# Performance work log

Measured on AMD Instinct MI355X. Metric: run time of the kernel, lower is better.

The kernel has to match this reference:

```python
import jax, jax.numpy as jnp
import numpy as np

B, L, DIM, H = 1, 2048, 1536, 24
HD = DIM // H  # head_dim = 64
EPS = 1e-6


def _rmsnorm(x, g):
    # RMSNorm over last dim with learnable scale (matches RMSNorm with elementwise_affine=True)
    return x * jax.lax.rsqrt(jnp.mean(x * x, axis=-1, keepdims=True) + EPS) * g


def setup_inputs() -> dict:
    key = jax.random.key(0)
    ks = jax.random.split(key, 4)
    s = 0.02
    return {
        "x": jax.random.normal(ks[0], (B, L, DIM), jnp.float32),
        "w_qkv": jax.random.normal(ks[1], (3 * DIM, DIM), jnp.float32) * s,
        "b_qkv": jnp.zeros((3 * DIM,), jnp.float32),
        "w_proj": jax.random.normal(ks[2], (DIM, DIM), jnp.float32) * s,
        "b_proj": jnp.zeros((DIM,), jnp.float32),
        "g_q": jnp.ones((HD,), jnp.float32),
        "g_k": jnp.ones((HD,), jnp.float32),
    }


def reference(x, w_qkv, b_qkv, w_proj, b_proj, g_q, g_k):
    Bb, Ll, C = x.shape
    # fused QKV projection: [B,L,C] -> [B,L,3C] -> [B,L,3,H,HD]
    qkv = (x @ w_qkv.T + b_qkv).reshape(Bb, Ll, 3, H, HD)
    q, k, v = qkv[:, :, 0], qkv[:, :, 1], qkv[:, :, 2]  # each [B,L,H,HD]
    # per-head RMS norm on q/k (qk_norm='rms')
    q = _rmsnorm(q, g_q)
    k = _rmsnorm(k, g_k)
    # scaled dot-product attention (torch SDPA default scale = 1/sqrt(head_dim))
    scale = 1.0 / np.sqrt(HD).astype(np.float32)
    scores = jnp.einsum('bqhd,bkhd->bhqk', q, k) * scale  # [B,H,L,L]
    attn = jax.nn.softmax(scores, axis=-1)
    o = jnp.einsum('bhqk,bkhd->bqhd', attn, v).reshape(Bb, Ll, C)
    # output projection
    return o @ w_proj.T + b_proj
```

## Files before the change

### kernel.cpp

```cpp
#include <hip/hip_runtime.h>
#include <stdint.h>

#define L_SEQ 2048
#define DIM 1536
#define NH 24
#define HD 64
#define NQKV 4608

typedef unsigned short u16;
typedef __attribute__((ext_vector_type(4))) float f32x4;
typedef __attribute__((ext_vector_type(8))) short bf16x8;
typedef __attribute__((ext_vector_type(4))) u16 u16x4;
typedef __attribute__((ext_vector_type(8))) u16 u16x8;

__device__ __forceinline__ u16 f2bf(float f) {
  unsigned u = __builtin_bit_cast(unsigned, f);
  u += 0x7fffu + ((u >> 16) & 1u);
  return (u16)(u >> 16);
}
__device__ __forceinline__ float b2f(u16 u) {
  return __builtin_bit_cast(float, (unsigned)u << 16);
}
__device__ __forceinline__ unsigned cvt_pk_bf16(float lo, float hi) {
  unsigned r;
  asm("v_cvt_pk_bf16_f32 %0, %1, %2" : "=v"(r) : "v"(lo), "v"(hi));
  return r;
}

__device__ __forceinline__ void gload_lds16(const void* g, void* lds) {
  __builtin_amdgcn_global_load_lds(
      (const __attribute__((address_space(1))) unsigned int*)g,
      (__attribute__((address_space(3))) unsigned int*)lds, 16, 0, 0);
}

__global__ __launch_bounds__(256) void cast3_kernel(const float* __restrict__ x,
                                                    const float* __restrict__ wq,
                                                    const float* __restrict__ wp,
                                                    u16* __restrict__ out) {
  const int n1 = (L_SEQ * DIM) / 4;
  const int n2 = (NQKV * DIM) / 4;
  const int n3 = (DIM * DIM) / 4;
  const int tot = n1 + n2 + n3;
  for (int i = blockIdx.x * 256 + threadIdx.x; i < tot; i += gridDim.x * 256) {
    const f32x4* src;
    int j;
    if (i < n1) {
      src = (const f32x4*)x;
      j = i;
    } else if (i < n1 + n2) {
      src = (const f32x4*)wq;
      j = i - n1;
    } else {
      src = (const f32x4*)wp;
      j = i - n1 - n2;
    }
    f32x4 v = src[j];
    u16x4 o;
    o.x = f2bf(v.x);
    o.y = f2bf(v.y);
    o.z = f2bf(v.z);
    o.w = f2bf(v.w);
    ((u16x4*)out)[i] = o;
  }
}

template <int WRITE_BF16, int BN>
__global__ __launch_bounds__(256) void gemm_bt(const u16* __restrict__ A,
                                               const u16* __restrict__ B,
                                               const float* __restrict__ bias,
                                               void* __restrict__ Cout,
                                               int M, int N, int K) {
  constexpr int NT = BN / 64 * 2;
  __shared__ u16 As[2][128 * 32];
  __shared__ u16 Bs[2][BN * 32];
  const int mb = M >> 7;
  const int f = (int)blockIdx.x;
  const int f2 = (f & 7) * ((int)gridDim.x >> 3) + (f >> 3);
  const int bx = f2 / mb;
  const int by = f2 % mb;
  const int tid = threadIdx.x;
  const int lane = tid & 63;
  const int l4 = lane & 15;
  const int wv = tid >> 6;
  const int wr = wv >> 1, wc = wv & 1;

  f32x4 acc[4][NT];
#pragma unroll
  for (int i = 0; i < 4; i++)
#pragma unroll
    for (int j = 0; j < NT; j++) acc[i][j] = (f32x4)(0.0f);

  const int e0 = tid * 8;
  const int r0 = e0 >> 5, c0 = e0 & 31;
  const u16* Ag0 = A + (size_t)(by * 128 + r0) * K + c0;
  const u16* Ag1 = A + (size_t)(by * 128 + r0 + 64) * K + c0;
  const u16* Bg0 = B + (size_t)(bx * BN + r0) * K + c0;
  const u16* Bg1 = B + (size_t)(bx * BN + r0 + 64) * K + c0;
  const int kc = (lane >> 4) * 8;
  const int wb = wv * 1024;

  gload_lds16(Ag0, (char*)As[0] + wb);
  gload_lds16(Ag1, (char*)As[0] + wb + 4096);
  gload_lds16(Bg0, (char*)Bs[0] + wb);
  if (BN == 128) gload_lds16(Bg1, (char*)Bs[0] + wb + 4096);
  __syncthreads();

  int cur = 0;
  for (int k0 = 0; k0 < K; k0 += 32) {
    const int nxt = cur ^ 1;
    if (k0 + 32 < K) {
      gload_lds16(Ag0 + k0 + 32, (char*)As[nxt] + wb);
      gload_lds16(Ag1 + k0 + 32, (char*)As[nxt] + wb + 4096);
      gload_lds16(Bg0 + k0 + 32, (char*)Bs[nxt] + wb);
      if (BN == 128) gload_lds16(Bg1 + k0 + 32, (char*)Bs[nxt] + wb + 4096);
    }
    const u16* Asc = As[cur];
    const u16* Bsc = Bs[cur];
    bf16x8 af[4], bfr[NT];
#pragma unroll
    for (int mt = 0; mt < 4; mt++)
      af[mt] = *(const bf16x8*)&Asc[(wr * 64 + mt * 16 + l4) * 32 + kc];
#pragma unroll
    for (int nt = 0; nt < NT; nt++)
      bfr[nt] = *(const bf16x8*)&Bsc[(wc * (BN / 2) + nt * 16 + l4) * 32 + kc];
#pragma unroll
    for (int mt = 0; mt < 4; mt++)
#pragma unroll
      for (int nt = 0; nt < NT; nt++)
        acc[mt][nt] = __builtin_amdgcn_mfma_f32_16x16x32_bf16(af[mt], bfr[nt],
                                                              acc[mt][nt], 0, 0, 0);
    __syncthreads();
    cur = nxt;
  }

  const int colb = bx * BN + wc * (BN / 2) + l4;
  const int rowb = by * 128 + wr * 64 + ((lane >> 4) << 2);
#pragma unroll
  for (int nt = 0; nt < NT; nt++) {
    const int col = colb + nt * 16;
    const float bv = bias[col];
#pragma unroll
    for (int mt = 0; mt < 4; mt++) {
#pragma unroll
      for (int r = 0; r < 4; r++) {
        const int row = rowb + mt * 16 + r;
        float v = acc[mt][nt][r] + bv;
        if (WRITE_BF16)
          ((u16*)Cout)[(size_t)row * N + col] = f2bf(v);
        else
          ((float*)Cout)[(size_t)row * N + col] = v;
      }
    }
  }
}

__global__ __launch_bounds__(256) void qkvnorm_kernel(const u16* __restrict__ qkv,
                                                      const float* __restrict__ gq,
                                                      const float* __restrict__ gk,
                                                      u16* __restrict__ Qh,
                                                      u16* __restrict__ Kh,
                                                      u16* __restrict__ Vt) {
  const int h = blockIdx.y;
  const int lblk = blockIdx.x * 64;
  const int tid = threadIdx.x;
  const int lane = tid & 63, wv = tid >> 6;
  __shared__ u16 vt[64][64];
  const float gqv = gq[lane] * 0.125f * 1.44269504088896f;
  const float gkv = gk[lane];
#pragma unroll 1
  for (int i = 0; i < 16; i++) {
    const int l = lblk + wv * 16 + i;
    const size_t base = (size_t)l * NQKV + h * HD + lane;
    const float q = b2f(qkv[base]);
    const float k = b2f(qkv[base + DIM]);
    float sq = q * q, sk = k * k;
#pragma unroll
    for (int m = 32; m; m >>= 1) {
      sq += __shfl_xor(sq, m);
      sk += __shfl_xor(sk, m);
    }
    const float rq = rsqrtf(sq * (1.0f / 64.0f) + 1e-6f);
    const float rk = rsqrtf(sk * (1.0f / 64.0f) + 1e-6f);
    const size_t ho = ((size_t)h * L_SEQ + l) * HD + lane;
    Qh[ho] = f2bf(q * rq * gqv);
    Kh[ho] = f2bf(k * rk * gkv);
    vt[wv * 16 + i][lane] = qkv[base + 2 * DIM];
  }
  __syncthreads();
  const int d = tid >> 2;
  const int cb = (tid & 3) * 16;
  u16* dst = Vt + ((size_t)h * HD + d) * L_SEQ + lblk + cb;
#pragma unroll
  for (int j0 = 0; j0 < 4; j0++) {
    u16x4 o;
    o.x = vt[cb + j0 * 4 + 0][d];
    o.y = vt[cb + j0 * 4 + 1][d];
    o.z = vt[cb + j0 * 4 + 2][d];
    o.w = vt[cb + j0 * 4 + 3][d];
    *(u16x4*)(dst + j0 * 4) = o;
  }
}

__global__ __launch_bounds__(256) void flash_kernel(const u16* __restrict__ Qh,
                                                    const u16* __restrict__ Kh,
                                                    const u16* __restrict__ Vt,
                                                    u16* __restrict__ O) {
  const int f = (int)blockIdx.y * (L_SEQ / 64) + (int)blockIdx.x;
  const int f2 = (f & 7) * 96 + (f >> 3);
  const int h = f2 >> 5;
  const int qblk = (f2 & 31) * 64;
  const int tid = threadIdx.x;
  const int lane = tid & 63, wv = tid >> 6;
  __shared__ u16 Ks[64][64];
  __shared__ u16 Vs[64][64];
  __shared__ u16 Ps[4][16][64];

  const int l4 = lane & 15;
  const int g = lane >> 4;
  const int kc = g * 8;
  const int swz = (l4 & 7) << 3;

  const int qrow = qblk + wv * 16 + l4;
  const u16* Qp = Qh + ((size_t)h * L_SEQ + qrow) * HD;
  const bf16x8 qf0 = *(const bf16x8*)(Qp + kc);
  const bf16x8 qf1 = *(const bf16x8*)(Qp + 32 + kc);
  const bf16x8 ones = (bf16x8)(short)0x3F80;

  f32x4 oacc[4];
#pragma unroll
  for (int dt = 0; dt < 4; dt++) oacc[dt] = (f32x4)(0.0f);
  float mr = -1e30f;
  float lr[4] = {0.f, 0.f, 0.f, 0.f};

  const int krow = tid >> 3;
  const int kcol = (tid & 7) * 8;
  const u16* Kg = Kh + (size_t)h * L_SEQ * HD + (size_t)krow * HD + kcol;
  u16* KsW0 = &Ks[krow][kcol ^ ((krow & 7) << 3)];
  u16* KsW1 = KsW0 + 32 * 64;
  const int vd = tid >> 2;
  const int vcol = (tid & 3) * 16;
  const u16* Vg = Vt + ((size_t)h * HD + vd) * L_SEQ;
  u16* VsW0 = &Vs[vd][vcol ^ ((vd & 7) << 3)];
  u16* VsW1 = &Vs[vd][(vcol + 8) ^ ((vd & 7) << 3)];

  bf16x8 kr0 = *(const bf16x8*)(Kg);
  bf16x8 kr1 = *(const bf16x8*)(Kg + 32 * HD);
  bf16x8 vr0 = *(const bf16x8*)(Vg + vcol);
  bf16x8 vr1 = *(const bf16x8*)(Vg + vcol + 8);

  for (int kb = 0; kb < L_SEQ; kb += 64) {
    __syncthreads();
    *(bf16x8*)KsW0 = kr0;
    *(bf16x8*)KsW1 = kr1;
    *(bf16x8*)VsW0 = vr0;
    *(bf16x8*)VsW1 = vr1;
    if (kb + 64 < L_SEQ) {
      kr0 = *(const bf16x8*)(Kg + (size_t)(kb + 64) * HD);
      kr1 = *(const bf16x8*)(Kg + (size_t)(kb + 96) * HD);
      vr0 = *(const bf16x8*)(Vg + kb + 64 + vcol);
      vr1 = *(const bf16x8*)(Vg + kb + 72 + vcol);
    }
    __syncthreads();

    f32x4 s[4];
    __builtin_amdgcn_s_setprio(1);
#pragma unroll
    for (int st = 0; st < 4; st++) {
      const u16* kp = &Ks[st * 16 + l4][0];
      bf16x8 ka = *(const bf16x8*)(kp + (kc ^ swz));
      bf16x8 kb2 = *(const bf16x8*)(kp + ((kc + 32) ^ swz));
      s[st] = __builtin_amdgcn_mfma_f32_16x16x32_bf16(ka, qf0, (f32x4)(0.0f), 0, 0, 0);
      s[st] = __builtin_amdgcn_mfma_f32_16x16x32_bf16(kb2, qf1, s[st], 0, 0, 0);
    }
    __builtin_amdgcn_s_setprio(0);

    float mx = fmaxf(fmaxf(s[0][0], s[0][1]), fmaxf(s[0][2], s[0][3]));
    mx = fmaxf(fmaxf(mx, s[1][0]), fmaxf(s[1][1], s[1][2]));
    mx = fmaxf(fmaxf(mx, s[1][3]), fmaxf(s[2][0], s[2][1]));
    mx = fmaxf(fmaxf(mx, s[2][2]), fmaxf(s[2][3], s[3][0]));
    mx = fmaxf(fmaxf(mx, s[3][1]), fmaxf(s[3][2], s[3][3]));
    mx = fmaxf(mx, __shfl_xor(mx, 16));
    mx = fmaxf(mx, __shfl_xor(mx, 32));

    if (__any(mx > mr + 8.0f)) {
      const float nm = fmaxf(mr, mx);
      const float sclo = __builtin_amdgcn_exp2f(mr - nm);
      mr = nm;
      float scl[4];
#pragma unroll
      for (int r = 0; r < 4; r++) scl[r] = __shfl(sclo, g * 4 + r);
#pragma unroll
      for (int r = 0; r < 4; r++) lr[r] *= scl[r];
#pragma unroll
      for (int dt = 0; dt < 4; dt++)
#pragma unroll
        for (int r = 0; r < 4; r++) oacc[dt][r] *= scl[r];
    }

    u16* pr = &Ps[wv][l4][0];
#pragma unroll
    for (int st = 0; st < 4; st++) {
      uint2 pw;
      pw.x = cvt_pk_bf16(__builtin_amdgcn_exp2f(s[st][0] - mr),
                         __builtin_amdgcn_exp2f(s[st][1] - mr));
      pw.y = cvt_pk_bf16(__builtin_amdgcn_exp2f(s[st][2] - mr),
                         __builtin_amdgcn_exp2f(s[st][3] - mr));
      *(uint2*)(pr + ((st * 16 + g * 4) ^ swz)) = pw;
    }

    const u16* pp = &Ps[wv][l4][0];
    bf16x8 pf0 = *(const bf16x8*)(pp + (kc ^ swz));
    bf16x8 pf1 = *(const bf16x8*)(pp + ((kc + 32) ^ swz));
    __builtin_amdgcn_s_setprio(1);
    f32x4 ls = __builtin_amdgcn_mfma_f32_16x16x32_bf16(pf0, ones, (f32x4)(0.0f), 0, 0, 0);
    ls = __builtin_amdgcn_mfma_f32_16x16x32_bf16(pf1, ones, ls, 0, 0, 0);
#pragma unroll
    for (int dt = 0; dt < 4; dt++) {
      const u16* vp = &Vs[dt * 16 + l4][0];
      bf16x8 vf0 = *(const bf16x8*)(vp + (kc ^ swz));
      bf16x8 vf1 = *(const bf16x8*)(vp + ((kc + 32) ^ swz));
      oacc[dt] = __builtin_amdgcn_mfma_f32_16x16x32_bf16(pf0, vf0, oacc[dt], 0, 0, 0);
      oacc[dt] = __builtin_amdgcn_mfma_f32_16x16x32_bf16(pf1, vf1, oacc[dt], 0, 0, 0);
    }
    __builtin_amdgcn_s_setprio(0);
#pragma unroll
    for (int r = 0; r < 4; r++) lr[r] += ls[r];
  }

#pragma unroll
  for (int r = 0; r < 4; r++) {
    const float inv = 1.0f / lr[r];
    const int row = qblk + wv * 16 + g * 4 + r;
#pragma unroll
    for (int dt = 0; dt < 4; dt++) {
      const int col = h * HD + dt * 16 + l4;
      O[(size_t)row * DIM + col] = f2bf(oacc[dt][r] * inv);
    }
  }
}

extern "C" void kernel_launch(void* const* d_in, const int* in_sizes, int n_in,
                              void* d_out, int out_size, void* d_ws, size_t ws_size,
                              hipStream_t stream) {
  const float* x = (const float*)d_in[0];
  const float* w_qkv = (const float*)d_in[1];
  const float* b_qkv = (const float*)d_in[2];
  const float* w_proj = (const float*)d_in[3];
  const float* b_proj = (const float*)d_in[4];
  const float* g_q = (const float*)d_in[5];
  const float* g_k = (const float*)d_in[6];

  char* ws = (char*)d_ws;
  u16* x_b = (u16*)(ws + 0);
  u16* wqkv_b = (u16*)(ws + 6291456);
  u16* wpj_b = (u16*)(ws + 20447232);
  u16* qkv = (u16*)(ws + 25165824);
  u16* Qh = (u16*)(ws + 44040192);
  u16* Kh = (u16*)(ws + 50331648);
  u16* Vt = (u16*)(ws + 56623104);
  u16* Ob = (u16*)(ws + 62914560);

  cast3_kernel<<<3072, 256, 0, stream>>>(x, w_qkv, w_proj, x_b);

  gemm_bt<1, 128><<<(L_SEQ / 128) * (NQKV / 128), 256, 0, stream>>>(
      x_b, wqkv_b, b_qkv, (void*)qkv, L_SEQ, NQKV, DIM);

  qkvnorm_kernel<<<dim3(L_SEQ / 64, NH), 256, 0, stream>>>(qkv, g_q, g_k, Qh, Kh, Vt);

  flash_kernel<<<dim3(L_SEQ / 64, NH), 256, 0, stream>>>(Qh, Kh, Vt, Ob);

  gemm_bt<0, 64><<<(L_SEQ / 128) * (DIM / 64), 256, 0, stream>>>(
      Ob, wpj_b, b_proj, d_out, L_SEQ, DIM, DIM);
}
```

Measured before the change: 146.1 us.

## Double-buffer K/V tiles in LDS and use one barrier per iteration

The flash attention kernel now keeps two LDS buffers for the K and V tiles. While the current tile is being used for compute, the next tile is written into the other buffer and the tile after it is prefetched into registers. This removes one of the two __syncthreads per key block and overlaps LDS stores with MFMA work. LDS use rises from about 24KB to about 40KB per block, which may lower occupancy.

```diff
diff --git a/kernel.cpp b/kernel.cpp
--- a/kernel.cpp
+++ b/kernel.cpp
@@ -211,9 +211,9 @@
   const int qblk = (f2 & 31) * 64;
   const int tid = threadIdx.x;
   const int lane = tid & 63, wv = tid >> 6;
-  __shared__ u16 Ks[64][64];
-  __shared__ u16 Vs[64][64];
-  __shared__ u16 Ps[4][16][64];
+  __shared__ u16 Ks[2 * 64 * 64];
+  __shared__ u16 Vs[2 * 64 * 64];
+  __shared__ u16 Ps[4 * 16 * 64];
 
   const int l4 = lane & 15;
   const int g = lane >> 4;
@@ -235,38 +235,51 @@
   const int krow = tid >> 3;
   const int kcol = (tid & 7) * 8;
   const u16* Kg = Kh + (size_t)h * L_SEQ * HD + (size_t)krow * HD + kcol;
-  u16* KsW0 = &Ks[krow][kcol ^ ((krow & 7) << 3)];
+  u16* KsW0 = &Ks[krow * 64 + (kcol ^ ((krow & 7) << 3))];
   u16* KsW1 = KsW0 + 32 * 64;
   const int vd = tid >> 2;
   const int vcol = (tid & 3) * 16;
   const u16* Vg = Vt + ((size_t)h * HD + vd) * L_SEQ;
-  u16* VsW0 = &Vs[vd][vcol ^ ((vd & 7) << 3)];
-  u16* VsW1 = &Vs[vd][(vcol + 8) ^ ((vd & 7) << 3)];
+  u16* VsW0 = &Vs[vd * 64 + (vcol ^ ((vd & 7) << 3))];
+  u16* VsW1 = &Vs[vd * 64 + ((vcol + 8) ^ ((vd & 7) << 3))];
 
   bf16x8 kr0 = *(const bf16x8*)(Kg);
   bf16x8 kr1 = *(const bf16x8*)(Kg + 32 * HD);
   bf16x8 vr0 = *(const bf16x8*)(Vg + vcol);
   bf16x8 vr1 = *(const bf16x8*)(Vg + vcol + 8);
-
+  *(bf16x8*)KsW0 = kr0;
+  *(bf16x8*)KsW1 = kr1;
+  *(bf16x8*)VsW0 = vr0;
+  *(bf16x8*)VsW1 = vr1;
+  kr0 = *(const bf16x8*)(Kg + (size_t)64 * HD);
+  kr1 = *(const bf16x8*)(Kg + (size_t)96 * HD);
+  vr0 = *(const bf16x8*)(Vg + 64 + vcol);
+  vr1 = *(const bf16x8*)(Vg + 64 + vcol + 8);
+  __syncthreads();
+
+  int cur = 0;
   for (int kb = 0; kb < L_SEQ; kb += 64) {
-    __syncthreads();
-    *(bf16x8*)KsW0 = kr0;
-    *(bf16x8*)KsW1 = kr1;
-    *(bf16x8*)VsW0 = vr0;
-    *(bf16x8*)VsW1 = vr1;
     if (kb + 64 < L_SEQ) {
-      kr0 = *(const bf16x8*)(Kg + (size_t)(kb + 64) * HD);
-      kr1 = *(const bf16x8*)(Kg + (size_t)(kb + 96) * HD);
-      vr0 = *(const bf16x8*)(Vg + kb + 64 + vcol);
-      vr1 = *(const bf16x8*)(Vg + kb + 72 + vcol);
-    }
-    __syncthreads();
+      const int bo = (cur ^ 1) * 4096;
+      *(bf16x8*)(KsW0 + bo) = kr0;
+      *(bf16x8*)(KsW1 + bo) = kr1;
+      *(bf16x8*)(VsW0 + bo) = vr0;
+      *(bf16x8*)(VsW1 + bo) = vr1;
+      if (kb + 128 < L_SEQ) {
+        kr0 = *(const bf16x8*)(Kg + (size_t)(kb + 128) * HD);
+        kr1 = *(const bf16x8*)(Kg + (size_t)(kb + 160) * HD);
+        vr0 = *(const bf16x8*)(Vg + kb + 128 + vcol);
+        vr1 = *(const bf16x8*)(Vg + kb + 128 + vcol + 8);
+      }
+    }
+    const u16* Kc = &Ks[cur * 4096];
+    const u16* Vc = &Vs[cur * 4096];
 
     f32x4 s[4];
     __builtin_amdgcn_s_setprio(1);
 #pragma unroll
     for (int st = 0; st < 4; st++) {
-      const u16* kp = &Ks[st * 16 + l4][0];
+      const u16* kp = Kc + (st * 16 + l4) * 64;
       bf16x8 ka = *(const bf16x8*)(kp + (kc ^ swz));
       bf16x8 kb2 = *(const bf16x8*)(kp + ((kc + 32) ^ swz));
       s[st] = __builtin_amdgcn_mfma_f32_16x16x32_bf16(ka, qf0, (f32x4)(0.0f), 0, 0, 0);
@@ -297,7 +310,7 @@
         for (int r = 0; r < 4; r++) oacc[dt][r] *= scl[r];
     }
 
-    u16* pr = &Ps[wv][l4][0];
+    u16* pr = &Ps[wv * 1024 + l4 * 64];
 #pragma unroll
     for (int st = 0; st < 4; st++) {
       uint2 pw;
@@ -308,7 +321,7 @@
       *(uint2*)(pr + ((st * 16 + g * 4) ^ swz)) = pw;
     }
 
-    const u16* pp = &Ps[wv][l4][0];
+    const u16* pp = &Ps[wv * 1024 + l4 * 64];
     bf16x8 pf0 = *(const bf16x8*)(pp + (kc ^ swz));
     bf16x8 pf1 = *(const bf16x8*)(pp + ((kc + 32) ^ swz));
     __builtin_amdgcn_s_setprio(1);
@@ -316,7 +329,7 @@
     ls = __builtin_amdgcn_mfma_f32_16x16x32_bf16(pf1, ones, ls, 0, 0, 0);
 #pragma unroll
     for (int dt = 0; dt < 4; dt++) {
-      const u16* vp = &Vs[dt * 16 + l4][0];
+      const u16* vp = Vc + (dt * 16 + l4) * 64;
       bf16x8 vf0 = *(const bf16x8*)(vp + (kc ^ swz));
       bf16x8 vf1 = *(const bf16x8*)(vp + ((kc + 32) ^ swz));
       oacc[dt] = __builtin_amdgcn_mfma_f32_16x16x32_bf16(pf0, vf0, oacc[dt], 0, 0, 0);
@@ -325,6 +338,9 @@
     __builtin_amdgcn_s_setprio(0);
 #pragma unroll
     for (int r = 0; r < 4; r++) lr[r] += ls[r];
+
+    __syncthreads();
+    cur ^= 1;
   }
 
 #pragma unroll
```

Result: no change. 146.2 us (+0.0%).
